# Performance work log

Hardware: AMD Instinct MI355X
Metric: run time of the kernel (lower is better)

Reference implementation:

```python
import jax, jax.numpy as jnp
import numpy as np


def setup_inputs() -> dict:
    key = jax.random.key(0)
    k1, k2 = jax.random.split(key)
    STATE_LEN, SEQ_LEN, HIDDEN = 8192, 8192, 1024
    out_state = jax.random.normal(k1, (STATE_LEN, HIDDEN), dtype=jnp.float32)
    history = jax.random.normal(k2, (SEQ_LEN, HIDDEN), dtype=jnp.float32)
    return {"out_state": out_state, "history": history}


def reference(out_state, history):
    # attn_energies[i, j] = dot(out_state[i], history[j])  ->  single GEMM
    energies = jnp.einsum('ih,jh->ij', out_state, history)  # [state_len, seq_len]
    # legacy F.softmax on a 2D tensor normalizes along dim=1 (the seq_len axis)
    return jax.nn.softmax(energies, axis=-1)
```

## Files before the change

### kernel.cpp

```cpp
#include <hip/hip_runtime.h>
#include <hip/hip_bf16.h>

#define M 8192
#define N 8192
#define K 1024
#define BM 256
#define BN 256
#define BK 32
#define KT (K/BK)

typedef __attribute__((ext_vector_type(8))) short short8;
typedef __attribute__((ext_vector_type(4))) float f32x4;

__device__ inline short f2bf(float x){
    __hip_bfloat16 h = __float2bfloat16(x);
    short s; __builtin_memcpy(&s, &h, 2); return s;
}
__device__ inline float bf2f(short s){
    __hip_bfloat16 h; __builtin_memcpy(&h, &s, 2);
    return __bfloat162float(h);
}

__device__ inline void conv8(float4 x0, float4 x1, short8& hi, short8& lo){
    float xs[8] = {x0.x,x0.y,x0.z,x0.w,x1.x,x1.y,x1.z,x1.w};
    #pragma unroll
    for (int j=0;j<8;++j){
        short h = f2bf(xs[j]);
        float r = xs[j] - bf2f(h);
        hi[j] = h; lo[j] = f2bf(r);
    }
}

#define GLOAD_LDS16(gp, lp) \
    __builtin_amdgcn_global_load_lds((const __attribute__((address_space(1))) void*)(gp), \
                                     (__attribute__((address_space(3))) void*)(lp), 16, 0, 0)

__global__ __launch_bounds__(512) void presplit_t(
    const float* __restrict__ A, const float* __restrict__ B,
    short* __restrict__ Aht, short* __restrict__ Alt,
    short* __restrict__ Bht, short* __restrict__ Blt)
{
    size_t c = (size_t)blockIdx.x * 512 + threadIdx.x;
    const float* src; short *dh, *dl;
    const size_t perMat = (size_t)M * (K/8);
    if (c < perMat){ src = A; dh = Aht; dl = Alt; }
    else { c -= perMat; src = B; dh = Bht; dl = Blt; }
    int row = (int)(c >> 7);
    int k8  = (int)(c & 127);
    const float* p = src + (size_t)row * K + k8 * 8;
    float4 x0 = *(const float4*)p;
    float4 x1 = *(const float4*)(p + 4);
    short8 hi, lo; conv8(x0, x1, hi, lo);
    size_t o = ((size_t)k8 * M + row) * 8;
    *(short8*)(dh + o) = hi;
    *(short8*)(dl + o) = lo;
}

__global__ __launch_bounds__(512, 2)
void gemm_t(const short* __restrict__ Aht, const short* __restrict__ Alt,
            const short* __restrict__ Bht, const short* __restrict__ Blt,
            float* __restrict__ C)
{
    __shared__ __align__(16) short lds[2][4][4][BM][8];

    const int tid  = threadIdx.x;
    const int lane = tid & 63, wid = tid >> 6;

    const int xcd = blockIdx.x & 7;
    const int gid = xcd * 128 + (blockIdx.x >> 3);
    const int bm0 = (gid >> 5) * BM;
    const int bn0 = (gid & 31) * BN;

    const int wr = wid >> 2, wc = wid & 3;
    const int fr = lane & 15, fg = lane >> 4;

    const int arr = wid >> 1;
    const short* gp = (arr == 0) ? Aht : (arr == 1) ? Alt : (arr == 2) ? Bht : Blt;
    const int   gb  = (arr < 2) ? bm0 : bn0;
    const int sbase = (wid & 1) * 2;

    f32x4 acc[8][4] = {};

    auto STAGE = [&](int buf, int kt){
        #pragma unroll
        for (int i = 0; i < 8; ++i){
            int s  = sbase + (i >> 2);
            int rb = i & 3;
            const short* src = gp + (((size_t)(kt * 4 + s)) * M + gb + rb * 64 + lane) * 8;
            GLOAD_LDS16(src, &lds[buf][arr][s][rb * 64][0]);
        }
    };

    STAGE(0, 0);
    __syncthreads();
    int cur = 0;

    for (int kt = 0; kt < KT; ++kt){
        if (kt + 1 < KT) STAGE(cur ^ 1, kt + 1);

        short8 ah[8], al[8], bh[4], bl[4];
        #pragma unroll
        for (int m = 0; m < 8; ++m){
            int row = wr * 128 + m * 16 + fr;
            ah[m] = *(const short8*)&lds[cur][0][fg][row][0];
            al[m] = *(const short8*)&lds[cur][1][fg][row][0];
        }
        #pragma unroll
        for (int n = 0; n < 4; ++n){
            int row = wc * 64 + n * 16 + fr;
            bh[n] = *(const short8*)&lds[cur][2][fg][row][0];
            bl[n] = *(const short8*)&lds[cur][3][fg][row][0];
        }

        __builtin_amdgcn_s_setprio(1);
        #pragma unroll
        for (int m = 0; m < 8; ++m){
            #pragma unroll
            for (int n = 0; n < 4; ++n){
                acc[m][n] = __builtin_amdgcn_mfma_f32_16x16x32_bf16(ah[m], bh[n], acc[m][n], 0, 0, 0);
                acc[m][n] = __builtin_amdgcn_mfma_f32_16x16x32_bf16(ah[m], bl[n], acc[m][n], 0, 0, 0);
                acc[m][n] = __builtin_amdgcn_mfma_f32_16x16x32_bf16(al[m], bh[n], acc[m][n], 0, 0, 0);
            }
        }
        __builtin_amdgcn_s_setprio(0);

        __syncthreads();
        cur ^= 1;
    }

    #pragma unroll
    for (int m = 0; m < 8; ++m){
        int grow = bm0 + wr * 128 + m * 16 + fg * 4;
        #pragma unroll
        for (int r = 0; r < 4; ++r){
            float* crow = C + (size_t)(grow + r) * N + bn0 + wc * 64 + fr;
            #pragma unroll
            for (int n = 0; n < 4; ++n)
                crow[n * 16] = acc[m][n][r];
        }
    }
}

#define FBM 128
#define FBN 128
#define FBK 64
#define FARR (FBM*FBK)
__global__ __launch_bounds__(256, 2)
void gemm_fb(const float* __restrict__ A, const float* __restrict__ B,
             float* __restrict__ C)
{
    __shared__ __align__(16) short sAh[FARR];
    __shared__ __align__(16) short sAl[FARR];
    __shared__ __align__(16) short sBh[FARR];
    __shared__ __align__(16) short sBl[FARR];

    const int tid  = threadIdx.x;
    const int lane = tid & 63, wid = tid >> 6;
    const int bm0 = blockIdx.y * FBM, bn0 = blockIdx.x * FBN;
    const int wr = wid >> 1, wc = wid & 1;
    const int fr = lane & 15, fg = lane >> 4;

    f32x4 acc[4][4] = {};

    for (int kt = 0; kt < K/FBK; ++kt){
        #pragma unroll
        for (int i = 0; i < 4; ++i){
            int s = tid + i * 256;
            int row = s >> 3, sp = s & 7;
            int widx = row * FBK + ((sp ^ (row & 7)) << 3);
            const float* ga = A + (size_t)(bm0 + row) * K + kt * FBK + sp * 8;
            float4 a0 = *(const float4*)ga, a1 = *(const float4*)(ga + 4);
            short8 hi, lo;
            conv8(a0, a1, hi, lo);
            *(short8*)&sAh[widx] = hi;
            *(short8*)&sAl[widx] = lo;
            const float* gbp = B + (size_t)(bn0 + row) * K + kt * FBK + sp * 8;
            float4 b0 = *(const float4*)gbp, b1 = *(const float4*)(gbp + 4);
            conv8(b0, b1, hi, lo);
            *(short8*)&sBh[widx] = hi;
            *(short8*)&sBl[widx] = lo;
        }
        __syncthreads();

        #pragma unroll
        for (int ks = 0; ks < 2; ++ks){
            short8 ah[4], al[4], bh[4], bl[4];
            #pragma unroll
            for (int m = 0; m < 4; ++m){
                int row = wr * 64 + m * 16 + fr;
                int idx = row * FBK + ((((ks << 2) | fg) ^ (row & 7)) << 3);
                ah[m] = *(const short8*)&sAh[idx];
                al[m] = *(const short8*)&sAl[idx];
            }
            #pragma unroll
            for (int n = 0; n < 4; ++n){
                int row = wc * 64 + n * 16 + fr;
                int idx = row * FBK + ((((ks << 2) | fg) ^ (row & 7)) << 3);
                bh[n] = *(const short8*)&sBh[idx];
                bl[n] = *(const short8*)&sBl[idx];
            }
            #pragma unroll
            for (int m = 0; m < 4; ++m){
                #pragma unroll
                for (int n = 0; n < 4; ++n){
                    acc[m][n] = __builtin_amdgcn_mfma_f32_16x16x32_bf16(ah[m], bh[n], acc[m][n], 0, 0, 0);
                    acc[m][n] = __builtin_amdgcn_mfma_f32_16x16x32_bf16(ah[m], bl[n], acc[m][n], 0, 0, 0);
                    acc[m][n] = __builtin_amdgcn_mfma_f32_16x16x32_bf16(al[m], bh[n], acc[m][n], 0, 0, 0);
                }
            }
        }
        __syncthreads();
    }

    #pragma unroll
    for (int m = 0; m < 4; ++m){
        int grow = bm0 + wr * 64 + m * 16 + fg * 4;
        #pragma unroll
        for (int r = 0; r < 4; ++r){
            float* crow = C + (size_t)(grow + r) * N + bn0 + wc * 64 + fr;
            #pragma unroll
            for (int n = 0; n < 4; ++n)
                crow[n * 16] = acc[m][n][r];
        }
    }
}

__global__ __launch_bounds__(256) void softmax_fused(float* __restrict__ E)
{
    const int row = blockIdx.x;
    const int tid = threadIdx.x;
    const int lane = tid & 63, wid = tid >> 6;
    float4* rp = (float4*)(E + (size_t)row * N);
    float4 v[8];
    float mx = -3.4e38f;
    #pragma unroll
    for (int i = 0; i < 8; ++i){
        v[i] = rp[tid + i * 256];
        mx = fmaxf(mx, fmaxf(fmaxf(v[i].x, v[i].y), fmaxf(v[i].z, v[i].w)));
    }
    #pragma unroll
    for (int off = 32; off; off >>= 1) mx = fmaxf(mx, __shfl_xor(mx, off));
    __shared__ float redm[4], reds[4];
    if (lane == 0) redm[wid] = mx;
    __syncthreads();
    mx = fmaxf(fmaxf(redm[0], redm[1]), fmaxf(redm[2], redm[3]));
    float s = 0.f;
    #pragma unroll
    for (int i = 0; i < 8; ++i){
        v[i].x = __expf(v[i].x - mx); v[i].y = __expf(v[i].y - mx);
        v[i].z = __expf(v[i].z - mx); v[i].w = __expf(v[i].w - mx);
        s += v[i].x + v[i].y + v[i].z + v[i].w;
    }
    #pragma unroll
    for (int off = 32; off; off >>= 1) s += __shfl_xor(s, off);
    if (lane == 0) reds[wid] = s;
    __syncthreads();
    float inv = 1.0f / (reds[0] + reds[1] + reds[2] + reds[3]);
    #pragma unroll
    for (int i = 0; i < 8; ++i){
        float4 o = v[i];
        o.x *= inv; o.y *= inv; o.z *= inv; o.w *= inv;
        rp[tid + i * 256] = o;
    }
}

extern "C" void kernel_launch(void* const* d_in, const int* in_sizes, int n_in,
                              void* d_out, int out_size, void* d_ws, size_t ws_size,
                              hipStream_t stream)
{
    const float* A = (const float*)d_in[0];
    const float* B = (const float*)d_in[1];
    float* out = (float*)d_out;

    const size_t elems = (size_t)M * K;
    const size_t splitBytes = 4 * elems * sizeof(short);

    if (ws_size >= splitBytes){
        short* Aht = (short*)d_ws;
        short* Alt = Aht + elems;
        short* Bht = Alt + elems;
        short* Blt = Bht + elems;
        presplit_t<<<4096, 512, 0, stream>>>(A, B, Aht, Alt, Bht, Blt);
        gemm_t<<<(M/BM)*(N/BN), 512, 0, stream>>>(Aht, Alt, Bht, Blt, out);
    } else {
        gemm_fb<<<dim3(N/FBN, M/FBM), 256, 0, stream>>>(A, B, out);
    }
    softmax_fused<<<M, 256, 0, stream>>>(out);
}
```

Measured before the change: 453.8 us.

## Split GEMM k-step into four phases interleaving LDS reads, prefetch and MFMA

Restructures the main GEMM loop so each k-tile runs in four phases. Each phase loads two A fragment rows from LDS, issues part of the next tile's global-to-LDS prefetch, then runs the MFMAs, with explicit barriers, waitcnts and sched_barriers between phases. B fragments are loaded once per tile, and the last iteration is peeled so it skips staging. The aim is to overlap LDS reads and global loads with matrix math and lower register pressure from holding all A fragments at once. The trade-off is extra workgroup barriers per tile and a schedule constrained by hand.

```diff
diff --git a/kernel.cpp b/kernel.cpp
--- a/kernel.cpp
+++ b/kernel.cpp
@@ -80,10 +80,12 @@
     const int sbase = (wid & 1) * 2;
 
     f32x4 acc[8][4] = {};
-
-    auto STAGE = [&](int buf, int kt){
-        #pragma unroll
-        for (int i = 0; i < 8; ++i){
+    short8 bh[4], bl[4];
+
+    auto STAGE2 = [&](int buf, int kt, int i0){
+        #pragma unroll
+        for (int ii = 0; ii < 2; ++ii){
+            int i  = i0 + ii;
             int s  = sbase + (i >> 2);
             int rb = i & 3;
             const short* src = gp + (((size_t)(kt * 4 + s)) * M + gb + rb * 64 + lane) * 8;
@@ -91,42 +93,60 @@
         }
     };
 
-    STAGE(0, 0);
+    int cur = 0;
+
+    #pragma unroll
+    for (int i0 = 0; i0 < 8; i0 += 2) STAGE2(0, 0, i0);
     __syncthreads();
-    int cur = 0;
-
-    for (int kt = 0; kt < KT; ++kt){
-        if (kt + 1 < KT) STAGE(cur ^ 1, kt + 1);
-
-        short8 ah[8], al[8], bh[4], bl[4];
-        #pragma unroll
-        for (int m = 0; m < 8; ++m){
-            int row = wr * 128 + m * 16 + fr;
-            ah[m] = *(const short8*)&lds[cur][0][fg][row][0];
-            al[m] = *(const short8*)&lds[cur][1][fg][row][0];
-        }
-        #pragma unroll
-        for (int n = 0; n < 4; ++n){
-            int row = wc * 64 + n * 16 + fr;
-            bh[n] = *(const short8*)&lds[cur][2][fg][row][0];
-            bl[n] = *(const short8*)&lds[cur][3][fg][row][0];
-        }
-
-        __builtin_amdgcn_s_setprio(1);
-        #pragma unroll
-        for (int m = 0; m < 8; ++m){
+
+    auto KSTEP = [&](int kt, bool doStage){
+        #pragma unroll
+        for (int p = 0; p < 4; ++p){
+            if (p == 0){
+                #pragma unroll
+                for (int n = 0; n < 4; ++n){
+                    int row = wc * 64 + n * 16 + fr;
+                    bh[n] = *(const short8*)&lds[cur][2][fg][row][0];
+                    bl[n] = *(const short8*)&lds[cur][3][fg][row][0];
+                }
+            }
+            int r0 = wr * 128 + (2 * p) * 16 + fr;
+            short8 ah0 = *(const short8*)&lds[cur][0][fg][r0][0];
+            short8 al0 = *(const short8*)&lds[cur][1][fg][r0][0];
+            short8 ah1 = *(const short8*)&lds[cur][0][fg][r0 + 16][0];
+            short8 al1 = *(const short8*)&lds[cur][1][fg][r0 + 16][0];
+
+            if (doStage && p < 2){
+                STAGE2(cur ^ 1, kt + 1, p * 4);
+                STAGE2(cur ^ 1, kt + 1, p * 4 + 2);
+            }
+
+            __builtin_amdgcn_s_barrier();
+            asm volatile("s_waitcnt lgkmcnt(0)" ::: "memory");
+            __builtin_amdgcn_sched_barrier(0);
+
+            __builtin_amdgcn_s_setprio(1);
             #pragma unroll
             for (int n = 0; n < 4; ++n){
-                acc[m][n] = __builtin_amdgcn_mfma_f32_16x16x32_bf16(ah[m], bh[n], acc[m][n], 0, 0, 0);
-                acc[m][n] = __builtin_amdgcn_mfma_f32_16x16x32_bf16(ah[m], bl[n], acc[m][n], 0, 0, 0);
-                acc[m][n] = __builtin_amdgcn_mfma_f32_16x16x32_bf16(al[m], bh[n], acc[m][n], 0, 0, 0);
-            }
-        }
-        __builtin_amdgcn_s_setprio(0);
-
-        __syncthreads();
+                acc[2*p  ][n] = __builtin_amdgcn_mfma_f32_16x16x32_bf16(ah0, bh[n], acc[2*p  ][n], 0, 0, 0);
+                acc[2*p  ][n] = __builtin_amdgcn_mfma_f32_16x16x32_bf16(ah0, bl[n], acc[2*p  ][n], 0, 0, 0);
+                acc[2*p  ][n] = __builtin_amdgcn_mfma_f32_16x16x32_bf16(al0, bh[n], acc[2*p  ][n], 0, 0, 0);
+                acc[2*p+1][n] = __builtin_amdgcn_mfma_f32_16x16x32_bf16(ah1, bh[n], acc[2*p+1][n], 0, 0, 0);
+                acc[2*p+1][n] = __builtin_amdgcn_mfma_f32_16x16x32_bf16(ah1, bl[n], acc[2*p+1][n], 0, 0, 0);
+                acc[2*p+1][n] = __builtin_amdgcn_mfma_f32_16x16x32_bf16(al1, bh[n], acc[2*p+1][n], 0, 0, 0);
+            }
+            __builtin_amdgcn_s_setprio(0);
+
+            if (p == 3)
+                asm volatile("s_waitcnt vmcnt(0)" ::: "memory");
+            __builtin_amdgcn_s_barrier();
+        }
+        __builtin_amdgcn_sched_barrier(0);
         cur ^= 1;
-    }
+    };
+
+    for (int kt = 0; kt < KT - 1; ++kt) KSTEP(kt, true);
+    KSTEP(KT - 1, false);
 
     #pragma unroll
     for (int m = 0; m < 8; ++m){
```

Result: slower. 463.4 us (+2.1%).

## Switch GEMM to 32x32 MFMA with 4-stage LDS pipeline and split phases

Applied to the files above, without the earlier changes.

Replaces the 16x16x32 bf16 MFMA tiles with 32x32x16 MFMAs and halves BK to 16. The double-buffered LDS becomes a four-slot ring that prefetches two k-steps ahead. Each iteration is split into two ping-pong phases that interleave LDS reads, async global-to-LDS staging and MFMA bursts, separated by explicit s_barrier and waitcnt instructions instead of __syncthreads. The aim is to hide global latency and cut register pressure and barrier stalls. The cost is more barriers per unit of work and fragile hand-tuned vmcnt counts.

```diff
diff --git a/kernel.cpp b/kernel.cpp
--- a/kernel.cpp
+++ b/kernel.cpp
@@ -6,11 +6,14 @@
 #define K 1024
 #define BM 256
 #define BN 256
-#define BK 32
+#define BK 16
 #define KT (K/BK)
 
 typedef __attribute__((ext_vector_type(8))) short short8;
 typedef __attribute__((ext_vector_type(4))) float f32x4;
+typedef __attribute__((ext_vector_type(16))) float f32x16;
+
+#define MFMA32(a,b,c) __builtin_amdgcn_mfma_f32_32x32x16_bf16((a),(b),(c),0,0,0)
 
 __device__ inline short f2bf(float x){
     __hip_bfloat16 h = __float2bfloat16(x);
@@ -61,7 +64,7 @@
             const short* __restrict__ Bht, const short* __restrict__ Blt,
             float* __restrict__ C)
 {
-    __shared__ __align__(16) short lds[2][4][4][BM][8];
+    __shared__ __align__(16) short lds[4][4][2][BM][8];
 
     const int tid  = threadIdx.x;
     const int lane = tid & 63, wid = tid >> 6;
@@ -72,71 +75,116 @@
     const int bn0 = (gid & 31) * BN;
 
     const int wr = wid >> 2, wc = wid & 3;
-    const int fr = lane & 15, fg = lane >> 4;
+    const int fr = lane & 31;
+    const int fg = lane >> 5;
 
     const int arr = wid >> 1;
     const short* gp = (arr == 0) ? Aht : (arr == 1) ? Alt : (arr == 2) ? Bht : Blt;
     const int   gb  = (arr < 2) ? bm0 : bn0;
-    const int sbase = (wid & 1) * 2;
-
-    f32x4 acc[8][4] = {};
-
-    auto STAGE = [&](int buf, int kt){
-        #pragma unroll
-        for (int i = 0; i < 8; ++i){
-            int s  = sbase + (i >> 2);
-            int rb = i & 3;
-            const short* src = gp + (((size_t)(kt * 4 + s)) * M + gb + rb * 64 + lane) * 8;
-            GLOAD_LDS16(src, &lds[buf][arr][s][rb * 64][0]);
+    const int   sl  = wid & 1;
+
+    f32x16 acc[4][2] = {};
+
+    auto STAGE2 = [&](int buf, int kt, int i0){
+        #pragma unroll
+        for (int ii = 0; ii < 2; ++ii){
+            int i = i0 + ii;
+            const short* src = gp + (((size_t)(kt * 2 + sl)) * M + gb + i * 64 + lane) * 8;
+            GLOAD_LDS16(src, &lds[buf][arr][sl][i * 64][0]);
         }
     };
 
-    STAGE(0, 0);
-    __syncthreads();
-    int cur = 0;
+    STAGE2(0, 0, 0); STAGE2(0, 0, 2);
+    STAGE2(1, 1, 0); STAGE2(1, 1, 2);
+    STAGE2(2, 2, 0); STAGE2(2, 2, 2);
+    asm volatile("s_waitcnt vmcnt(8)" ::: "memory");
+    __builtin_amdgcn_s_barrier();
 
     for (int kt = 0; kt < KT; ++kt){
-        if (kt + 1 < KT) STAGE(cur ^ 1, kt + 1);
-
-        short8 ah[8], al[8], bh[4], bl[4];
-        #pragma unroll
-        for (int m = 0; m < 8; ++m){
-            int row = wr * 128 + m * 16 + fr;
-            ah[m] = *(const short8*)&lds[cur][0][fg][row][0];
-            al[m] = *(const short8*)&lds[cur][1][fg][row][0];
-        }
-        #pragma unroll
-        for (int n = 0; n < 4; ++n){
-            int row = wc * 64 + n * 16 + fr;
-            bh[n] = *(const short8*)&lds[cur][2][fg][row][0];
-            bl[n] = *(const short8*)&lds[cur][3][fg][row][0];
-        }
-
+        const int cur = kt & 3;
+        const int nxt = (kt + 2) & 3;
+        const bool doStage = (kt < KT - 2);
+
+        short8 bh0, bl0, bh1, bl1, ah0, al0, ah1, al1;
+        {
+            int rb0 = wc * 64 + fr, rb1 = wc * 64 + 32 + fr;
+            bh0 = *(const short8*)&lds[cur][2][fg][rb0][0];
+            bl0 = *(const short8*)&lds[cur][3][fg][rb0][0];
+            bh1 = *(const short8*)&lds[cur][2][fg][rb1][0];
+            bl1 = *(const short8*)&lds[cur][3][fg][rb1][0];
+            int r0 = wr * 128 + fr;
+            ah0 = *(const short8*)&lds[cur][0][fg][r0][0];
+            al0 = *(const short8*)&lds[cur][1][fg][r0][0];
+            ah1 = *(const short8*)&lds[cur][0][fg][r0 + 32][0];
+            al1 = *(const short8*)&lds[cur][1][fg][r0 + 32][0];
+        }
+        if (doStage) STAGE2(nxt, kt + 2, 0);
+
+        __builtin_amdgcn_s_barrier();
+        asm volatile("s_waitcnt lgkmcnt(0)" ::: "memory");
+        __builtin_amdgcn_sched_barrier(0);
         __builtin_amdgcn_s_setprio(1);
-        #pragma unroll
-        for (int m = 0; m < 8; ++m){
-            #pragma unroll
-            for (int n = 0; n < 4; ++n){
-                acc[m][n] = __builtin_amdgcn_mfma_f32_16x16x32_bf16(ah[m], bh[n], acc[m][n], 0, 0, 0);
-                acc[m][n] = __builtin_amdgcn_mfma_f32_16x16x32_bf16(ah[m], bl[n], acc[m][n], 0, 0, 0);
-                acc[m][n] = __builtin_amdgcn_mfma_f32_16x16x32_bf16(al[m], bh[n], acc[m][n], 0, 0, 0);
+        acc[0][0] = MFMA32(ah0, bh0, acc[0][0]);
+        acc[0][0] = MFMA32(ah0, bl0, acc[0][0]);
+        acc[0][0] = MFMA32(al0, bh0, acc[0][0]);
+        acc[0][1] = MFMA32(ah0, bh1, acc[0][1]);
+        acc[0][1] = MFMA32(ah0, bl1, acc[0][1]);
+        acc[0][1] = MFMA32(al0, bh1, acc[0][1]);
+        acc[1][0] = MFMA32(ah1, bh0, acc[1][0]);
+        acc[1][0] = MFMA32(ah1, bl0, acc[1][0]);
+        acc[1][0] = MFMA32(al1, bh0, acc[1][0]);
+        acc[1][1] = MFMA32(ah1, bh1, acc[1][1]);
+        acc[1][1] = MFMA32(ah1, bl1, acc[1][1]);
+        acc[1][1] = MFMA32(al1, bh1, acc[1][1]);
+        __builtin_amdgcn_s_setprio(0);
+        __builtin_amdgcn_s_barrier();
+
+        short8 ah2, al2, ah3, al3;
+        {
+            int r2 = wr * 128 + 64 + fr;
+            ah2 = *(const short8*)&lds[cur][0][fg][r2][0];
+            al2 = *(const short8*)&lds[cur][1][fg][r2][0];
+            ah3 = *(const short8*)&lds[cur][0][fg][r2 + 32][0];
+            al3 = *(const short8*)&lds[cur][1][fg][r2 + 32][0];
+        }
+        if (doStage) STAGE2(nxt, kt + 2, 2);
+
+        __builtin_amdgcn_s_barrier();
+        asm volatile("s_waitcnt lgkmcnt(0)" ::: "memory");
+        __builtin_amdgcn_sched_barrier(0);
+        __builtin_amdgcn_s_setprio(1);
+        acc[2][0] = MFMA32(ah2, bh0, acc[2][0]);
+        acc[2][0] = MFMA32(ah2, bl0, acc[2][0]);
+        acc[2][0] = MFMA32(al2, bh0, acc[2][0]);
+        acc[2][1] = MFMA32(ah2, bh1, acc[2][1]);
+        acc[2][1] = MFMA32(ah2, bl1, acc[2][1]);
+        acc[2][1] = MFMA32(al2, bh1, acc[2][1]);
+        acc[3][0] = MFMA32(ah3, bh0, acc[3][0]);
+        acc[3][0] = MFMA32(ah3, bl0, acc[3][0]);
+        acc[3][0] = MFMA32(al3, bh0, acc[3][0]);
+        acc[3][1] = MFMA32(ah3, bh1, acc[3][1]);
+        acc[3][1] = MFMA32(ah3, bl1, acc[3][1]);
+        acc[3][1] = MFMA32(al3, bh1, acc[3][1]);
+        __builtin_amdgcn_s_setprio(0);
+
+        if (kt < KT - 2)       asm volatile("s_waitcnt vmcnt(4)" ::: "memory");
+        else if (kt == KT - 2) asm volatile("s_waitcnt vmcnt(0)" ::: "memory");
+        __builtin_amdgcn_s_barrier();
+    }
+
+    #pragma unroll
+    for (int m = 0; m < 4; ++m){
+        #pragma unroll
+        for (int n = 0; n < 2; ++n){
+            #pragma unroll
+            for (int g = 0; g < 4; ++g){
+                #pragma unroll
+                for (int r = 0; r < 4; ++r){
+                    int row = r + 8 * g + 4 * fg;
+                    C[(size_t)(bm0 + wr * 128 + m * 32 + row) * N
+                      + bn0 + wc * 64 + n * 32 + fr] = acc[m][n][g * 4 + r];
+                }
             }
-        }
-        __builtin_amdgcn_s_setprio(0);
-
-        __syncthreads();
-        cur ^= 1;
-    }
-
-    #pragma unroll
-    for (int m = 0; m < 8; ++m){
-        int grow = bm0 + wr * 128 + m * 16 + fg * 4;
-        #pragma unroll
-        for (int r = 0; r < 4; ++r){
-            float* crow = C + (size_t)(grow + r) * N + bn0 + wc * 64 + fr;
-            #pragma unroll
-            for (int n = 0; n < 4; ++n)
-                crow[n * 16] = acc[m][n][r];
         }
     }
 }
```

Result: slower. 487.6 us (+7.4%).

## Switch to 32x32 MFMA with 4-stage LDS pipeline and register prefetch

Applied to the files above, without the earlier changes.

Replaces the 16x16x32 bf16 MFMA tiles with 32x32x16 MFMA and halves BK to 16. Shared memory becomes a 4-deep ring buffer with explicit vmcnt waits and raw barriers instead of a double buffer with __syncthreads. The A fragments for the next k-step are read into a second register set while the current step's MFMAs run. The goal is to hide global-load and LDS latency and to cut LDS read traffic per MFMA. The cost is more register pressure and finer-grained iterations with more barriers.

```diff
diff --git a/kernel.cpp b/kernel.cpp
--- a/kernel.cpp
+++ b/kernel.cpp
@@ -6,11 +6,14 @@
 #define K 1024
 #define BM 256
 #define BN 256
-#define BK 32
+#define BK 16
 #define KT (K/BK)
 
 typedef __attribute__((ext_vector_type(8))) short short8;
 typedef __attribute__((ext_vector_type(4))) float f32x4;
+typedef __attribute__((ext_vector_type(16))) float f32x16;
+
+#define MFMA32(a,b,c) __builtin_amdgcn_mfma_f32_32x32x16_bf16((a),(b),(c),0,0,0)
 
 __device__ inline short f2bf(float x){
     __hip_bfloat16 h = __float2bfloat16(x);
@@ -61,7 +64,7 @@
             const short* __restrict__ Bht, const short* __restrict__ Blt,
             float* __restrict__ C)
 {
-    __shared__ __align__(16) short lds[2][4][4][BM][8];
+    __shared__ __align__(16) short lds[4][4][2][BM][8];
 
     const int tid  = threadIdx.x;
     const int lane = tid & 63, wid = tid >> 6;
@@ -72,73 +75,117 @@
     const int bn0 = (gid & 31) * BN;
 
     const int wr = wid >> 2, wc = wid & 3;
-    const int fr = lane & 15, fg = lane >> 4;
+    const int fr = lane & 31;
+    const int fg = lane >> 5;
 
     const int arr = wid >> 1;
     const short* gp = (arr == 0) ? Aht : (arr == 1) ? Alt : (arr == 2) ? Bht : Blt;
     const int   gb  = (arr < 2) ? bm0 : bn0;
-    const int sbase = (wid & 1) * 2;
-
-    f32x4 acc[8][4] = {};
+    const int   sl  = wid & 1;
+
+    f32x16 acc[4][2] = {};
 
     auto STAGE = [&](int buf, int kt){
         #pragma unroll
-        for (int i = 0; i < 8; ++i){
-            int s  = sbase + (i >> 2);
-            int rb = i & 3;
-            const short* src = gp + (((size_t)(kt * 4 + s)) * M + gb + rb * 64 + lane) * 8;
-            GLOAD_LDS16(src, &lds[buf][arr][s][rb * 64][0]);
+        for (int i = 0; i < 4; ++i){
+            const short* src = gp + (((size_t)(kt * 2 + sl)) * M + gb + i * 64 + lane) * 8;
+            GLOAD_LDS16(src, &lds[buf][arr][sl][i * 64][0]);
         }
     };
 
-    STAGE(0, 0);
-    __syncthreads();
-    int cur = 0;
-
-    for (int kt = 0; kt < KT; ++kt){
-        if (kt + 1 < KT) STAGE(cur ^ 1, kt + 1);
-
-        short8 ah[8], al[8], bh[4], bl[4];
-        #pragma unroll
-        for (int m = 0; m < 8; ++m){
-            int row = wr * 128 + m * 16 + fr;
-            ah[m] = *(const short8*)&lds[cur][0][fg][row][0];
-            al[m] = *(const short8*)&lds[cur][1][fg][row][0];
-        }
-        #pragma unroll
-        for (int n = 0; n < 4; ++n){
-            int row = wc * 64 + n * 16 + fr;
-            bh[n] = *(const short8*)&lds[cur][2][fg][row][0];
-            bl[n] = *(const short8*)&lds[cur][3][fg][row][0];
-        }
-
-        __builtin_amdgcn_s_setprio(1);
-        #pragma unroll
-        for (int m = 0; m < 8; ++m){
-            #pragma unroll
-            for (int n = 0; n < 4; ++n){
-                acc[m][n] = __builtin_amdgcn_mfma_f32_16x16x32_bf16(ah[m], bh[n], acc[m][n], 0, 0, 0);
-                acc[m][n] = __builtin_amdgcn_mfma_f32_16x16x32_bf16(ah[m], bl[n], acc[m][n], 0, 0, 0);
-                acc[m][n] = __builtin_amdgcn_mfma_f32_16x16x32_bf16(al[m], bh[n], acc[m][n], 0, 0, 0);
+    short8 ah0a, ah1a, ah2a, ah3a, al0a, al1a, al2a, al3a;
+    short8 ah0b, ah1b, ah2b, ah3b, al0b, al1b, al2b, al3b;
+    short8 bh0, bh1, bl0, bl1;
+
+    const int rA = wr * 128 + fr;
+    const int rB = wc * 64 + fr;
+
+    #define READ_B(buf) do { \
+        bh0 = *(const short8*)&lds[(buf)][2][fg][rB][0];      \
+        bl0 = *(const short8*)&lds[(buf)][3][fg][rB][0];      \
+        bh1 = *(const short8*)&lds[(buf)][2][fg][rB + 32][0]; \
+        bl1 = *(const short8*)&lds[(buf)][3][fg][rB + 32][0]; \
+    } while (0)
+
+    #define READ_A(S, buf) do { \
+        ah0##S = *(const short8*)&lds[(buf)][0][fg][rA][0];      \
+        al0##S = *(const short8*)&lds[(buf)][1][fg][rA][0];      \
+        ah1##S = *(const short8*)&lds[(buf)][0][fg][rA + 32][0]; \
+        al1##S = *(const short8*)&lds[(buf)][1][fg][rA + 32][0]; \
+        ah2##S = *(const short8*)&lds[(buf)][0][fg][rA + 64][0]; \
+        al2##S = *(const short8*)&lds[(buf)][1][fg][rA + 64][0]; \
+        ah3##S = *(const short8*)&lds[(buf)][0][fg][rA + 96][0]; \
+        al3##S = *(const short8*)&lds[(buf)][1][fg][rA + 96][0]; \
+    } while (0)
+
+    #define DO_MFMA(S) do { \
+        __builtin_amdgcn_s_setprio(1); \
+        acc[0][0] = MFMA32(ah0##S, bh0, acc[0][0]); \
+        acc[0][0] = MFMA32(ah0##S, bl0, acc[0][0]); \
+        acc[0][0] = MFMA32(al0##S, bh0, acc[0][0]); \
+        acc[0][1] = MFMA32(ah0##S, bh1, acc[0][1]); \
+        acc[0][1] = MFMA32(ah0##S, bl1, acc[0][1]); \
+        acc[0][1] = MFMA32(al0##S, bh1, acc[0][1]); \
+        acc[1][0] = MFMA32(ah1##S, bh0, acc[1][0]); \
+        acc[1][0] = MFMA32(ah1##S, bl0, acc[1][0]); \
+        acc[1][0] = MFMA32(al1##S, bh0, acc[1][0]); \
+        acc[1][1] = MFMA32(ah1##S, bh1, acc[1][1]); \
+        acc[1][1] = MFMA32(ah1##S, bl1, acc[1][1]); \
+        acc[1][1] = MFMA32(al1##S, bh1, acc[1][1]); \
+        acc[2][0] = MFMA32(ah2##S, bh0, acc[2][0]); \
+        acc[2][0] = MFMA32(ah2##S, bl0, acc[2][0]); \
+        acc[2][0] = MFMA32(al2##S, bh0, acc[2][0]); \
+        acc[2][1] = MFMA32(ah2##S, bh1, acc[2][1]); \
+        acc[2][1] = MFMA32(ah2##S, bl1, acc[2][1]); \
+        acc[2][1] = MFMA32(al2##S, bh1, acc[2][1]); \
+        acc[3][0] = MFMA32(ah3##S, bh0, acc[3][0]); \
+        acc[3][0] = MFMA32(ah3##S, bl0, acc[3][0]); \
+        acc[3][0] = MFMA32(al3##S, bh0, acc[3][0]); \
+        acc[3][1] = MFMA32(ah3##S, bh1, acc[3][1]); \
+        acc[3][1] = MFMA32(ah3##S, bl1, acc[3][1]); \
+        acc[3][1] = MFMA32(al3##S, bh1, acc[3][1]); \
+        __builtin_amdgcn_s_setprio(0); \
+    } while (0)
+
+    #define BODY(kt, CUR, NXT) do { \
+        if ((kt) + 2 < KT) asm volatile("s_waitcnt vmcnt(4)" ::: "memory"); \
+        else               asm volatile("s_waitcnt vmcnt(0)" ::: "memory"); \
+        __builtin_amdgcn_s_barrier(); \
+        if ((kt) + 3 < KT) STAGE(((kt) + 3) & 3, (kt) + 3); \
+        READ_B((kt) & 3); \
+        if ((kt) + 1 < KT) READ_A(NXT, ((kt) + 1) & 3); \
+        DO_MFMA(CUR); \
+    } while (0)
+
+    STAGE(0, 0); STAGE(1, 1); STAGE(2, 2);
+    asm volatile("s_waitcnt vmcnt(8)" ::: "memory");
+    __builtin_amdgcn_s_barrier();
+    READ_A(a, 0);
+
+    for (int kt = 0; kt < KT; kt += 2){
+        BODY(kt,     a, b);
+        BODY(kt + 1, b, a);
+    }
+
+    #pragma unroll
+    for (int m = 0; m < 4; ++m){
+        #pragma unroll
+        for (int n = 0; n < 2; ++n){
+            #pragma unroll
+            for (int g = 0; g < 4; ++g){
+                #pragma unroll
+                for (int r = 0; r < 4; ++r){
+                    int row = r + 8 * g + 4 * fg;
+                    C[(size_t)(bm0 + wr * 128 + m * 32 + row) * N
+                      + bn0 + wc * 64 + n * 32 + fr] = acc[m][n][g * 4 + r];
+                }
             }
         }
-        __builtin_amdgcn_s_setprio(0);
-
-        __syncthreads();
-        cur ^= 1;
-    }
-
-    #pragma unroll
-    for (int m = 0; m < 8; ++m){
-        int grow = bm0 + wr * 128 + m * 16 + fg * 4;
-        #pragma unroll
-        for (int r = 0; r < 4; ++r){
-            float* crow = C + (size_t)(grow + r) * N + bn0 + wc * 64 + fr;
-            #pragma unroll
-            for (int n = 0; n < 4; ++n)
-                crow[n * 16] = acc[m][n][r];
-        }
-    }
+    }
+    #undef BODY
+    #undef DO_MFMA
+    #undef READ_A
+    #undef READ_B
 }
 
 #define FBM 128
```

Result: slower. 482.6 us (+6.4%).
